# Performance work log

Hardware: AMD Instinct MI355X
Metric: run time of the kernel (lower is better)

The kernel has to match this reference:

```python
import jax, jax.numpy as jnp
import numpy as np
from jax import lax

ROUNDS = 64
HIDDEN = 256
BATCH = 16384


def setup_inputs() -> dict:
    key = jax.random.key(0)
    k1, k2, k3 = jax.random.split(key, 3)
    # state: (B, 256) bits in {0,1} as float32 (output of bytes_to_bits)
    state = jax.random.bernoulli(k1, 0.5, (BATCH, HIDDEN)).astype(jnp.float32)
    # matrices: (64, 256, 256) ternary values in {-1,0,1} (byte % 3 - 1)
    matrices = jax.random.randint(k2, (ROUNDS, HIDDEN, HIDDEN), -1, 2).astype(jnp.float32)
    # noise: (B, 64, 256) bits in {0,1} derived from sha256 of the nonce
    noise = jax.random.bernoulli(k3, 0.5, (BATCH, ROUNDS, HIDDEN)).astype(jnp.float32)
    return {"state": state, "matrices": matrices, "noise": noise}


def reference(state, matrices, noise):
    # 64-round recurrence: s <- (floor(s @ M_r^T + n_r)) mod 2
    noise_r = jnp.transpose(noise, (1, 0, 2))  # (R, B, H)

    def step(s, xs):
        M, n = xs  # M: (H,H), n: (B,H)
        s = jnp.remainder(jnp.floor(s @ M.T + n), 2.0)
        return s, None

    final, _ = lax.scan(step, state, (matrices, noise_r))
    return final  # (B, 256) bits as float32
```

## Files before the change

kernel.cpp:

```cpp
#include <hip/hip_runtime.h>

#define R_ROUNDS 64
#define HID 256
#define BATCH 16384
#define ROWS_PER_WAVE 4

__global__ void pack_matrices_kernel(const float* __restrict__ M,
                                     unsigned int* __restrict__ P) {
    const int e    = blockIdx.x * blockDim.x + threadIdx.x;
    const int lane = threadIdx.x & 63;
    const float v  = M[e];
    const unsigned long long m = __ballot(v != 0.0f);
    if (lane == 0) {
        const int w = e >> 5;
        P[w]     = (unsigned int)m;
        P[w + 1] = (unsigned int)(m >> 32);
    }
}

__global__ __launch_bounds__(256) void tenshash_kernel(
        const float* __restrict__ state,
        const unsigned int* __restrict__ pA,
        const float* __restrict__ noise,
        float* __restrict__ out) {
    const int lane = threadIdx.x & 63;
    const int wave = (blockIdx.x * blockDim.x + threadIdx.x) >> 6;
    const int row0 = wave * ROWS_PER_WAVE;

    unsigned long long S[ROWS_PER_WAVE][4];
#pragma unroll
    for (int rw = 0; rw < ROWS_PER_WAVE; ++rw) {
#pragma unroll
        for (int i = 0; i < 4; ++i) {
            const float v = state[(size_t)(row0 + rw) * HID + i * 64 + lane];
            S[rw][i] = __ballot(v != 0.0f);
        }
    }

#pragma unroll 1
    for (int r = 0; r < R_ROUNDS; ++r) {
        uint4 a[4][2];
        const uint4* pa = (const uint4*)(pA + (size_t)r * HID * 8);
#pragma unroll
        for (int i = 0; i < 4; ++i) {
            a[i][0] = pa[(i * 64 + lane) * 2];
            a[i][1] = pa[(i * 64 + lane) * 2 + 1];
        }

        float nf[ROWS_PER_WAVE][4];
#pragma unroll
        for (int rw = 0; rw < ROWS_PER_WAVE; ++rw) {
            const float* np = noise + (size_t)(row0 + rw) * (R_ROUNDS * HID)
                                    + (size_t)r * HID;
#pragma unroll
            for (int i = 0; i < 4; ++i) nf[rw][i] = np[i * 64 + lane];
        }

        unsigned long long NS[ROWS_PER_WAVE][4];
#pragma unroll
        for (int rw = 0; rw < ROWS_PER_WAVE; ++rw) {
            const unsigned int s0 = (unsigned int)(S[rw][0]);
            const unsigned int s1 = (unsigned int)(S[rw][0] >> 32);
            const unsigned int s2 = (unsigned int)(S[rw][1]);
            const unsigned int s3 = (unsigned int)(S[rw][1] >> 32);
            const unsigned int s4 = (unsigned int)(S[rw][2]);
            const unsigned int s5 = (unsigned int)(S[rw][2] >> 32);
            const unsigned int s6 = (unsigned int)(S[rw][3]);
            const unsigned int s7 = (unsigned int)(S[rw][3] >> 32);
#pragma unroll
            for (int i = 0; i < 4; ++i) {
                unsigned int c = __popc(a[i][0].x & s0) + __popc(a[i][0].y & s1)
                               + __popc(a[i][0].z & s2) + __popc(a[i][0].w & s3)
                               + __popc(a[i][1].x & s4) + __popc(a[i][1].y & s5)
                               + __popc(a[i][1].z & s6) + __popc(a[i][1].w & s7)
                               + (unsigned int)nf[rw][i];
                NS[rw][i] = __ballot((int)(c & 1u));
            }
        }
#pragma unroll
        for (int rw = 0; rw < ROWS_PER_WAVE; ++rw)
#pragma unroll
            for (int i = 0; i < 4; ++i) S[rw][i] = NS[rw][i];
    }

#pragma unroll
    for (int rw = 0; rw < ROWS_PER_WAVE; ++rw) {
#pragma unroll
        for (int i = 0; i < 4; ++i) {
            const unsigned int bit = (unsigned int)((S[rw][i] >> lane) & 1ULL);
            out[(size_t)(row0 + rw) * HID + i * 64 + lane] = (float)bit;
        }
    }
}

extern "C" void kernel_launch(void* const* d_in, const int* in_sizes, int n_in,
                              void* d_out, int out_size, void* d_ws, size_t ws_size,
                              hipStream_t stream) {
    const float* state = (const float*)d_in[0];
    const float* mats  = (const float*)d_in[1];
    const float* noise = (const float*)d_in[2];
    float* out         = (float*)d_out;
    unsigned int* pA   = (unsigned int*)d_ws;

    const int n_m = R_ROUNDS * HID * HID;
    pack_matrices_kernel<<<n_m / 256, 256, 0, stream>>>(mats, pA);

    const int waves  = BATCH / ROWS_PER_WAVE;
    const int blocks = waves / 4;
    tenshash_kernel<<<blocks, 256, 0, stream>>>(state, pA, noise, out);
}
```

Baseline: 249.0 us.

## Double-buffer round loads, vectorize noise/state/output to float4, and interleave hidden-bit layout

The main kernel now software-pipelines the round loop, prefetching the next round's packed matrix rows and noise into a second register buffer while the current round computes. The bit layout is changed so each lane handles hidden indices 4*lane..4*lane+3, which makes the state, noise and output accesses 16-byte float4 loads and stores. The pack kernel is rewritten to match, with one wave per matrix row and a float4 load per lane. In exchange, register pressure rises and launch bounds set a minimum occupancy, which could force spills.

```diff
diff --git a/kernel.cpp b/kernel.cpp
--- a/kernel.cpp
+++ b/kernel.cpp
@@ -1,95 +1,112 @@
 #include <hip/hip_runtime.h>
+
+typedef unsigned int u32;
+typedef unsigned long long u64;
 
 #define R_ROUNDS 64
 #define HID 256
 #define BATCH 16384
-#define ROWS_PER_WAVE 4
+#define RPW 4
 
-__global__ void pack_matrices_kernel(const float* __restrict__ M,
-                                     unsigned int* __restrict__ P) {
-    const int e    = blockIdx.x * blockDim.x + threadIdx.x;
+
+__global__ __launch_bounds__(256) void pack_matrices_kernel(
+        const float* __restrict__ M, u32* __restrict__ P) {
     const int lane = threadIdx.x & 63;
-    const float v  = M[e];
-    const unsigned long long m = __ballot(v != 0.0f);
-    if (lane == 0) {
-        const int w = e >> 5;
-        P[w]     = (unsigned int)m;
-        P[w + 1] = (unsigned int)(m >> 32);
+    const int row  = (int)((blockIdx.x * blockDim.x + threadIdx.x) >> 6);
+    const float4 v = *(const float4*)(M + (size_t)row * HID + 4 * lane);
+    const u64 b0 = __ballot(v.x != 0.0f);
+    const u64 b1 = __ballot(v.y != 0.0f);
+    const u64 b2 = __ballot(v.z != 0.0f);
+    const u64 b3 = __ballot(v.w != 0.0f);
+    if (lane < 8) {
+        const int i = lane >> 1;
+        u64 bb = b0;
+        if (i == 1) bb = b1;
+        if (i == 2) bb = b2;
+        if (i == 3) bb = b3;
+        P[row * 8 + lane] = (lane & 1) ? (u32)(bb >> 32) : (u32)bb;
     }
 }
 
-__global__ __launch_bounds__(256) void tenshash_kernel(
+__global__ __launch_bounds__(256, 4) void tenshash_kernel(
         const float* __restrict__ state,
-        const unsigned int* __restrict__ pA,
+        const u32*  __restrict__ pA,
         const float* __restrict__ noise,
         float* __restrict__ out) {
     const int lane = threadIdx.x & 63;
-    const int wave = (blockIdx.x * blockDim.x + threadIdx.x) >> 6;
-    const int row0 = wave * ROWS_PER_WAVE;
+    const int wave = (int)((blockIdx.x * blockDim.x + threadIdx.x) >> 6);
+    const int row0 = wave * RPW;
 
-    unsigned long long S[ROWS_PER_WAVE][4];
+    u64 S0[RPW], S1[RPW], S2[RPW], S3[RPW];
 #pragma unroll
-    for (int rw = 0; rw < ROWS_PER_WAVE; ++rw) {
-#pragma unroll
-        for (int i = 0; i < 4; ++i) {
-            const float v = state[(size_t)(row0 + rw) * HID + i * 64 + lane];
-            S[rw][i] = __ballot(v != 0.0f);
-        }
+    for (int rw = 0; rw < RPW; ++rw) {
+        const float4 v = *(const float4*)(state + (size_t)(row0 + rw) * HID + 4 * lane);
+        S0[rw] = __ballot(v.x != 0.0f);
+        S1[rw] = __ballot(v.y != 0.0f);
+        S2[rw] = __ballot(v.z != 0.0f);
+        S3[rw] = __ballot(v.w != 0.0f);
     }
 
-#pragma unroll 1
-    for (int r = 0; r < R_ROUNDS; ++r) {
-        uint4 a[4][2];
-        const uint4* pa = (const uint4*)(pA + (size_t)r * HID * 8);
+    const u32*   pA_l = pA + 32 * lane;
+    const float* no_l = noise + (size_t)row0 * (R_ROUNDS * HID) + 4 * lane;
+
+    uint4  aA[8], aB[8];
+    float4 nA[RPW], nB[RPW];
+
+    auto LOAD_A = [&](uint4* a, int r) {
+        const uint4* p = (const uint4*)(pA_l + r * (HID * 8));
 #pragma unroll
-        for (int i = 0; i < 4; ++i) {
-            a[i][0] = pa[(i * 64 + lane) * 2];
-            a[i][1] = pa[(i * 64 + lane) * 2 + 1];
-        }
-
-        float nf[ROWS_PER_WAVE][4];
+        for (int t = 0; t < 8; ++t) a[t] = p[t];
+    };
+    auto LOAD_N = [&](float4* n, int r) {
 #pragma unroll
-        for (int rw = 0; rw < ROWS_PER_WAVE; ++rw) {
-            const float* np = noise + (size_t)(row0 + rw) * (R_ROUNDS * HID)
-                                    + (size_t)r * HID;
+        for (int rw = 0; rw < RPW; ++rw)
+            n[rw] = *(const float4*)(no_l + (size_t)rw * (R_ROUNDS * HID) + r * HID);
+    };
+    auto COMPUTE = [&](const uint4* a, const float4* n) {
 #pragma unroll
-            for (int i = 0; i < 4; ++i) nf[rw][i] = np[i * 64 + lane];
-        }
-
-        unsigned long long NS[ROWS_PER_WAVE][4];
-#pragma unroll
-        for (int rw = 0; rw < ROWS_PER_WAVE; ++rw) {
-            const unsigned int s0 = (unsigned int)(S[rw][0]);
-            const unsigned int s1 = (unsigned int)(S[rw][0] >> 32);
-            const unsigned int s2 = (unsigned int)(S[rw][1]);
-            const unsigned int s3 = (unsigned int)(S[rw][1] >> 32);
-            const unsigned int s4 = (unsigned int)(S[rw][2]);
-            const unsigned int s5 = (unsigned int)(S[rw][2] >> 32);
-            const unsigned int s6 = (unsigned int)(S[rw][3]);
-            const unsigned int s7 = (unsigned int)(S[rw][3] >> 32);
+        for (int rw = 0; rw < RPW; ++rw) {
+            u64 ns0, ns1, ns2, ns3;
 #pragma unroll
             for (int i = 0; i < 4; ++i) {
-                unsigned int c = __popc(a[i][0].x & s0) + __popc(a[i][0].y & s1)
-                               + __popc(a[i][0].z & s2) + __popc(a[i][0].w & s3)
-                               + __popc(a[i][1].x & s4) + __popc(a[i][1].y & s5)
-                               + __popc(a[i][1].z & s6) + __popc(a[i][1].w & s7)
-                               + (unsigned int)nf[rw][i];
-                NS[rw][i] = __ballot((int)(c & 1u));
+                const u64 W0 = (u64)a[2 * i].x     | ((u64)a[2 * i].y     << 32);
+                const u64 W1 = (u64)a[2 * i].z     | ((u64)a[2 * i].w     << 32);
+                const u64 W2 = (u64)a[2 * i + 1].x | ((u64)a[2 * i + 1].y << 32);
+                const u64 W3 = (u64)a[2 * i + 1].z | ((u64)a[2 * i + 1].w << 32);
+                const float nfv = (i == 0) ? n[rw].x : (i == 1) ? n[rw].y
+                                : (i == 2) ? n[rw].z : n[rw].w;
+                const u32 c = (u32)__popcll(W0 & S0[rw]) + (u32)__popcll(W1 & S1[rw])
+                            + (u32)__popcll(W2 & S2[rw]) + (u32)__popcll(W3 & S3[rw])
+                            + (u32)nfv;
+                const u64 nb = __ballot((c & 1u) != 0);
+                if (i == 0) ns0 = nb; else if (i == 1) ns1 = nb;
+                else if (i == 2) ns2 = nb; else ns3 = nb;
             }
+            S0[rw] = ns0; S1[rw] = ns1; S2[rw] = ns2; S3[rw] = ns3;
         }
-#pragma unroll
-        for (int rw = 0; rw < ROWS_PER_WAVE; ++rw)
-#pragma unroll
-            for (int i = 0; i < 4; ++i) S[rw][i] = NS[rw][i];
+    };
+
+    LOAD_A(aA, 0);
+    LOAD_N(nA, 0);
+#pragma unroll 1
+    for (int r = 0; r < R_ROUNDS; r += 2) {
+        LOAD_A(aB, r + 1);
+        LOAD_N(nB, r + 1);
+        COMPUTE(aA, nA);
+        const int r2 = (r + 2 < R_ROUNDS) ? r + 2 : (R_ROUNDS - 1);
+        LOAD_A(aA, r2);
+        LOAD_N(nA, r2);
+        COMPUTE(aB, nB);
     }
 
 #pragma unroll
-    for (int rw = 0; rw < ROWS_PER_WAVE; ++rw) {
-#pragma unroll
-        for (int i = 0; i < 4; ++i) {
-            const unsigned int bit = (unsigned int)((S[rw][i] >> lane) & 1ULL);
-            out[(size_t)(row0 + rw) * HID + i * 64 + lane] = (float)bit;
-        }
+    for (int rw = 0; rw < RPW; ++rw) {
+        float4 o;
+        o.x = (float)((u32)(S0[rw] >> lane) & 1u);
+        o.y = (float)((u32)(S1[rw] >> lane) & 1u);
+        o.z = (float)((u32)(S2[rw] >> lane) & 1u);
+        o.w = (float)((u32)(S3[rw] >> lane) & 1u);
+        *(float4*)(out + (size_t)(row0 + rw) * HID + 4 * lane) = o;
     }
 }
 
@@ -100,12 +117,10 @@
     const float* mats  = (const float*)d_in[1];
     const float* noise = (const float*)d_in[2];
     float* out         = (float*)d_out;
-    unsigned int* pA   = (unsigned int*)d_ws;
+    u32* pA            = (u32*)d_ws;
 
-    const int n_m = R_ROUNDS * HID * HID;
-    pack_matrices_kernel<<<n_m / 256, 256, 0, stream>>>(mats, pA);
+    pack_matrices_kernel<<<(R_ROUNDS * HID) / 4, 256, 0, stream>>>(mats, pA);
 
-    const int waves  = BATCH / ROWS_PER_WAVE;
-    const int blocks = waves / 4;
+    const int blocks = (BATCH / RPW) / 4;
     tenshash_kernel<<<blocks, 256, 0, stream>>>(state, pA, noise, out);
 }
```

New measurement: 389.1 us. +56.3%, slower.
